# Performance work log

Hardware: AMD Instinct MI355X
Metric: run time of the kernel (lower is better)

Reference implementation:

```python
import jax, jax.numpy as jnp
import numpy as np

V, D, H = 32000, 512, 512
B, T, MAX_LEN = 32, 128, 48


def setup_inputs() -> dict:
    key = jax.random.key(0)
    ks = jax.random.split(key, 12)
    s = 0.02  # xavier-ish scale
    return {
        "inputs": jax.random.randint(ks[0], (B, 1), 0, V),
        "context": jax.random.normal(ks[1], (B, 1, H), dtype=jnp.float32),
        "max_len": MAX_LEN,
        "encoder_outputs": jax.random.normal(ks[2], (B, T, H), dtype=jnp.float32),
        "emb": jax.random.normal(ks[3], (V, D), dtype=jnp.float32) * s,
        "gru_Wih": jax.random.normal(ks[4], (3 * H, D + H), dtype=jnp.float32) * s,
        "gru_Whh": jax.random.normal(ks[5], (3 * H, H), dtype=jnp.float32) * s,
        "gru_bih": jax.random.normal(ks[6], (3 * H,), dtype=jnp.float32) * s,
        "gru_bhh": jax.random.normal(ks[7], (3 * H,), dtype=jnp.float32) * s,
        "lin_W": jax.random.normal(ks[8], (V, 2 * H), dtype=jnp.float32) * s,
        "lin_b": jax.random.normal(ks[9], (V,), dtype=jnp.float32) * s,
        "attn_W": jax.random.normal(ks[10], (H, H), dtype=jnp.float32) * s,
        "attn_b": jax.random.normal(ks[11], (H,), dtype=jnp.float32) * s,
    }


def reference(inputs, context, max_len, encoder_outputs, emb, gru_Wih, gru_Whh,
              gru_bih, gru_bhh, lin_W, lin_b, attn_W, attn_b):
    Bsz, Tlen, Hdim = encoder_outputs.shape
    ctx0 = context[:, 0, :]          # B,H  (last encoder hidden)
    e0 = emb[inputs[:, 0]]           # B,D  (start symbol embedding)
    h0 = jnp.zeros((Bsz, Hdim), dtype=context.dtype)
    # attn linear on encoder outputs is loop-invariant -> hoist
    energies = jnp.einsum('bth,gh->btg', encoder_outputs, attn_W) + attn_b  # B,T,H

    def gru_step(x, h):
        gi = x @ gru_Wih.T + gru_bih
        gh = h @ gru_Whh.T + gru_bhh
        ir, iz, inn = jnp.split(gi, 3, axis=-1)
        hr, hz, hn = jnp.split(gh, 3, axis=-1)
        r = jax.nn.sigmoid(ir + hr)
        z = jax.nn.sigmoid(iz + hz)
        n = jnp.tanh(inn + r * hn)
        return (1.0 - z) * n + z * h

    def step(carry, _):
        h, ctx, e = carry
        h = gru_step(jnp.concatenate([e, ctx], axis=-1), h)
        score = jnp.concatenate([h, ctx], axis=-1) @ lin_W.T + lin_b  # B,V
        logp = jax.nn.log_softmax(score, axis=-1)
        e_next = emb[jnp.argmax(logp, axis=-1)]                       # greedy feedback
        alpha = jax.nn.softmax(jnp.einsum('bth,bh->bt', energies, h), axis=-1)
        ctx_next = jnp.einsum('bt,bth->bh', alpha, encoder_outputs)
        return (h, ctx_next, e_next), logp

    _, logps = jax.lax.scan(step, (h0, ctx0, e0), None, length=max_len)
    # logps: (max_len, B, V) -> cat along dim1 then view => (B*max_len, V)
    return jnp.transpose(logps, (1, 0, 2)).reshape(Bsz * max_len, -1)
```

## Files before the change

### kernel.cpp

```cpp
#include <hip/hip_runtime.h>
#include <hip/hip_bf16.h>

#define V  32000
#define D  512
#define H  512
#define B  32
#define T  128
#define L  48
#define KLIN 1024
#define KGRU 1536
#define RESCUE_DELTA 0.04f
#define MAXCAND 16

typedef __attribute__((ext_vector_type(8))) short bf16x8;
typedef __attribute__((ext_vector_type(4))) float f32x4;

#define MFMA16(a, b, c) __builtin_amdgcn_mfma_f32_16x16x32_bf16(a, b, c, 0, 0, 0)

__device__ __forceinline__ void split1(float f, unsigned short* hi, unsigned short* lo) {
    unsigned u  = __float_as_uint(f);
    unsigned uh = u + (0x7FFFu + ((u >> 16) & 1u));
    unsigned short hs = (unsigned short)(uh >> 16);
    float hf = __uint_as_float(((unsigned)hs) << 16);
    float l  = f - hf;
    unsigned ul = __float_as_uint(l);
    ul += 0x7FFFu + ((ul >> 16) & 1u);
    *hi = hs;
    *lo = (unsigned short)(ul >> 16);
}

__device__ __forceinline__ void split8(const float* __restrict__ p, bf16x8& hi, bf16x8& lo) {
    float4 w0 = reinterpret_cast<const float4*>(p)[0];
    float4 w1 = reinterpret_cast<const float4*>(p)[1];
    float w[8] = {w0.x, w0.y, w0.z, w0.w, w1.x, w1.y, w1.z, w1.w};
    #pragma unroll
    for (int i = 0; i < 8; ++i) {
        unsigned u  = __float_as_uint(w[i]);
        unsigned uh = u + (0x7FFFu + ((u >> 16) & 1u));
        unsigned short hs = (unsigned short)(uh >> 16);
        float hf = __uint_as_float(((unsigned)hs) << 16);
        float l  = w[i] - hf;
        unsigned ul = __float_as_uint(l);
        ul += 0x7FFFu + ((ul >> 16) & 1u);
        hi[i] = (short)hs;
        lo[i] = (short)(ul >> 16);
    }
}

__device__ __forceinline__ void merge2(float& m1, int& i1, float& m2, int& i2,
                                       float om1, int oi1, float om2, int oi2) {
    bool ogt = (om1 > m1) || (om1 == m1 && oi1 < i1);
    float t1 = ogt ? om1 : m1; int ti1 = ogt ? oi1 : i1;
    float l1 = ogt ? m1 : om1; int li1 = ogt ? i1 : oi1;
    float w2 = ogt ? om2 : m2; int wi2 = ogt ? oi2 : i2;
    bool lgt = (l1 > w2) || (l1 == w2 && li1 < wi2);
    m1 = t1; i1 = ti1;
    m2 = lgt ? l1 : w2; i2 = lgt ? li1 : wi2;
}

__global__ void presplit_lin_hi(const float* __restrict__ src, unsigned short* __restrict__ hi)
{
    long i = (long)blockIdx.x * 256 + threadIdx.x;
    if (i >= (long)V * 128) return;
    bf16x8 h8, l8;
    split8(src + i * 8, h8, l8);
    *(bf16x8*)(hi + i * 8) = h8;
}

__global__ void presplit_gru(const float* __restrict__ Wih, const float* __restrict__ Whh,
                             unsigned short* __restrict__ hi, unsigned short* __restrict__ lo)
{
    int i = blockIdx.x * 256 + threadIdx.x;
    if (i >= 1536 * 192) return;
    int col = i / 192, k = (i % 192) * 8;
    const float* src = (k < 1024) ? (Wih + (size_t)col * 1024 + k)
                                  : (Whh + (size_t)col * 512 + (k - 1024));
    bf16x8 h8, l8;
    split8(src, h8, l8);
    *(bf16x8*)(hi + (size_t)col * KGRU + k) = h8;
    *(bf16x8*)(lo + (size_t)col * KGRU + k) = l8;
}

__global__ void init_state(const int* __restrict__ inputs, const float* __restrict__ context,
                           const float* __restrict__ emb, float* __restrict__ h_t,
                           unsigned short* __restrict__ Xghi, unsigned short* __restrict__ Xglo,
                           unsigned short* __restrict__ Xlhi, unsigned short* __restrict__ Xllo,
                           float* __restrict__ Xf)
{
    int idx = blockIdx.x * 256 + threadIdx.x;
    int b = idx >> 9, j = idx & 511;
    int tok = inputs[b];
    float e = emb[(size_t)tok * D + j];
    split1(e, &Xghi[b * KGRU + j], &Xglo[b * KGRU + j]);
    float c = context[b * H + j];
    split1(c, &Xghi[b * KGRU + 512 + j], &Xglo[b * KGRU + 512 + j]);
    split1(c, &Xlhi[b * KLIN + 512 + j], &Xllo[b * KLIN + 512 + j]);
    Xf[b * KLIN + 512 + j] = c;
    Xghi[b * KGRU + 1024 + j] = 0;
    Xglo[b * KGRU + 1024 + j] = 0;
    h_t[j * 32 + b] = 0.f;
}

__global__ void __launch_bounds__(256) energies_gemm(
    const float* __restrict__ enc, const float* __restrict__ attnW,
    const float* __restrict__ attnb, float* __restrict__ energies)
{
    int wave = threadIdx.x >> 6, lane = threadIdx.x & 63;
    int col = blockIdx.y * 64 + wave * 16 + (lane & 15);
    int kg  = (lane >> 4) * 8;
    int arow0 = blockIdx.x * 32 + (lane & 15);
    f32x4 acc0 = {0.f,0.f,0.f,0.f}, acc1 = {0.f,0.f,0.f,0.f};
    for (int k0 = 0; k0 < 512; k0 += 32) {
        bf16x8 bh, bl;   split8(attnW + (size_t)col * 512 + k0 + kg, bh, bl);
        bf16x8 a0h, a0l; split8(enc + (size_t)arow0 * 512 + k0 + kg, a0h, a0l);
        bf16x8 a1h, a1l; split8(enc + (size_t)(arow0 + 16) * 512 + k0 + kg, a1h, a1l);
        acc0 = MFMA16(a0h, bh, acc0);  acc1 = MFMA16(a1h, bh, acc1);
        acc0 = MFMA16(a0l, bh, acc0);  acc1 = MFMA16(a1l, bh, acc1);
        acc0 = MFMA16(a0h, bl, acc0);  acc1 = MFMA16(a1h, bl, acc1);
    }
    float bias = attnb[col];
    int r0 = (lane >> 4) * 4;
    #pragma unroll
    for (int i = 0; i < 4; ++i) {
        int row = blockIdx.x * 32 + r0 + i;
        energies[(size_t)row * 512 + col]        = acc0[i] + bias;
        energies[(size_t)(row + 16) * 512 + col] = acc1[i] + bias;
    }
}

__global__ void __launch_bounds__(384) gru_fused(
    const unsigned short* __restrict__ Ghi, const unsigned short* __restrict__ Glo,
    const unsigned short* __restrict__ Xghi_r, const unsigned short* __restrict__ Xglo_r,
    unsigned short* __restrict__ Xghi_w, unsigned short* __restrict__ Xglo_w,
    unsigned short* __restrict__ Xlhi_w, unsigned short* __restrict__ Xllo_w,
    float* __restrict__ Xf_w,
    const float* __restrict__ bih, const float* __restrict__ bhh,
    float* __restrict__ h_t)
{
    __shared__ float AI[3][32][16], AH[3][32][16];
    __shared__ float R[32][16], Z[32][16];
    int w = threadIdx.x >> 6, lane = threadIdx.x & 63;
    int g = (w < 3) ? w : w - 3;
    int half = (w >= 3) ? 1 : 0;
    int c = lane & 15, grp = lane >> 4, kg = grp * 8;
    int j = blockIdx.x * 16 + c;
    int gcol = g * 512 + j;
    const unsigned short* wh = Ghi + (size_t)gcol * KGRU;
    const unsigned short* wl = Glo + (size_t)gcol * KGRU;
    const unsigned short* xh = Xghi_r + (size_t)c * KGRU;
    const unsigned short* xl = Xglo_r + (size_t)c * KGRU;
    f32x4 aI0 = {0.f,0.f,0.f,0.f}, aI1 = {0.f,0.f,0.f,0.f};
    f32x4 aH0 = {0.f,0.f,0.f,0.f}, aH1 = {0.f,0.f,0.f,0.f};
    for (int k0 = half * 512; k0 < half * 512 + 512; k0 += 32) {
        bf16x8 bh = *(const bf16x8*)(wh + k0 + kg);
        bf16x8 bl = *(const bf16x8*)(wl + k0 + kg);
        bf16x8 a0h = *(const bf16x8*)(xh + k0 + kg);
        bf16x8 a0l = *(const bf16x8*)(xl + k0 + kg);
        bf16x8 a1h = *(const bf16x8*)(xh + 16 * KGRU + k0 + kg);
        bf16x8 a1l = *(const bf16x8*)(xl + 16 * KGRU + k0 + kg);
        aI0 = MFMA16(a0h, bh, aI0);  aI1 = MFMA16(a1h, bh, aI1);
        aI0 = MFMA16(a0l, bh, aI0);  aI1 = MFMA16(a1l, bh, aI1);
        aI0 = MFMA16(a0h, bl, aI0);  aI1 = MFMA16(a1h, bl, aI1);
    }
    for (int k0 = 1024 + half * 256; k0 < 1024 + half * 256 + 256; k0 += 32) {
        bf16x8 bh = *(const bf16x8*)(wh + k0 + kg);
        bf16x8 bl = *(const bf16x8*)(wl + k0 + kg);
        bf16x8 a0h = *(const bf16x8*)(xh + k0 + kg);
        bf16x8 a0l = *(const bf16x8*)(xl + k0 + kg);
        bf16x8 a1h = *(const bf16x8*)(xh + 16 * KGRU + k0 + kg);
        bf16x8 a1l = *(const bf16x8*)(xl + 16 * KGRU + k0 + kg);
        aH0 = MFMA16(a0h, bh, aH0);  aH1 = MFMA16(a1h, bh, aH1);
        aH0 = MFMA16(a0l, bh, aH0);  aH1 = MFMA16(a1l, bh, aH1);
        aH0 = MFMA16(a0h, bl, aH0);  aH1 = MFMA16(a1h, bl, aH1);
    }
    if (w >= 3) {
        #pragma unroll
        for (int i = 0; i < 4; ++i) {
            AI[g][grp * 4 + i][c] = aI0[i];  AI[g][grp * 4 + i + 16][c] = aI1[i];
            AH[g][grp * 4 + i][c] = aH0[i];  AH[g][grp * 4 + i + 16][c] = aH1[i];
        }
    }
    __syncthreads();
    float gi[8], gh[8];
    if (w < 3) {
        float bi = bih[gcol], bhv = bhh[gcol];
        #pragma unroll
        for (int i = 0; i < 4; ++i) {
            gi[i]     = aI0[i] + AI[g][grp * 4 + i][c]      + bi;
            gi[i + 4] = aI1[i] + AI[g][grp * 4 + i + 16][c] + bi;
            gh[i]     = aH0[i] + AH[g][grp * 4 + i][c]      + bhv;
            gh[i + 4] = aH1[i] + AH[g][grp * 4 + i + 16][c] + bhv;
        }
        if (w == 0) {
            #pragma unroll
            for (int i = 0; i < 8; ++i) {
                int b = (i < 4) ? grp * 4 + i : grp * 4 + (i - 4) + 16;
                R[b][c] = 1.f / (1.f + expf(-(gi[i] + gh[i])));
            }
        } else if (w == 1) {
            #pragma unroll
            for (int i = 0; i < 8; ++i) {
                int b = (i < 4) ? grp * 4 + i : grp * 4 + (i - 4) + 16;
                Z[b][c] = 1.f / (1.f + expf(-(gi[i] + gh[i])));
            }
        }
    }
    __syncthreads();
    if (w == 2) {
        float4 h0 = *(const float4*)(h_t + (size_t)j * 32 + grp * 4);
        float4 h1 = *(const float4*)(h_t + (size_t)j * 32 + grp * 4 + 16);
        float hold[8] = {h0.x, h0.y, h0.z, h0.w, h1.x, h1.y, h1.z, h1.w};
        float hn[8];
        #pragma unroll
        for (int i = 0; i < 8; ++i) {
            int b = (i < 4) ? grp * 4 + i : grp * 4 + (i - 4) + 16;
            float n = tanhf(gi[i] + R[b][c] * gh[i]);
            float z = Z[b][c];
            hn[i] = (1.f - z) * n + z * hold[i];
        }
        *(float4*)(h_t + (size_t)j * 32 + grp * 4)      = make_float4(hn[0], hn[1], hn[2], hn[3]);
        *(float4*)(h_t + (size_t)j * 32 + grp * 4 + 16) = make_float4(hn[4], hn[5], hn[6], hn[7]);
        #pragma unroll
        for (int i = 0; i < 8; ++i) {
            int b = (i < 4) ? grp * 4 + i : grp * 4 + (i - 4) + 16;
            split1(hn[i], &Xlhi_w[(size_t)b * KLIN + j], &Xllo_w[(size_t)b * KLIN + j]);
            Xf_w[(size_t)b * KLIN + j] = hn[i];
            split1(hn[i], &Xghi_w[(size_t)b * KGRU + 1024 + j], &Xglo_w[(size_t)b * KGRU + 1024 + j]);
        }
    }
}

__global__ void __launch_bounds__(256) score_attn(
    const unsigned short* __restrict__ Whi, const float* __restrict__ linb,
    const unsigned short* __restrict__ Xlhi_r, const unsigned short* __restrict__ Xllo_r,
    unsigned short* __restrict__ Xlhi_n, unsigned short* __restrict__ Xllo_n,
    float* __restrict__ Xf_n,
    unsigned short* __restrict__ Xghi_n, unsigned short* __restrict__ Xglo_n,
    const float* __restrict__ h_t, const float* __restrict__ energies,
    const float* __restrict__ enc,
    float* __restrict__ out,
    float* __restrict__ Pm, int* __restrict__ Pa,
    float* __restrict__ Pm2, int* __restrict__ Pa2,
    float* __restrict__ Ps, int t)
{
    __shared__ float Lm1[4][32], Lm2[4][32], Ls[4][32];
    __shared__ int   Li1[4][32], Li2[4][32];
    __shared__ float hrow[512], aw[128], red[256];
    int tid = threadIdx.x;
    if (blockIdx.x < 500) {
        int wave = tid >> 6, lane = tid & 63;
        int c = lane & 15, grp = lane >> 4, kg = grp * 8;
        int col = blockIdx.x * 64 + wave * 16 + c;
        const unsigned short* x0h = Xlhi_r + (size_t)c * KLIN + kg;
        const unsigned short* x0l = Xllo_r + (size_t)c * KLIN + kg;
        const unsigned short* whp = Whi + (size_t)col * KLIN + kg;
        f32x4 acc0 = {0.f,0.f,0.f,0.f}, acc1 = {0.f,0.f,0.f,0.f};
        #pragma unroll 4
        for (int k0 = 0; k0 < 1024; k0 += 32) {
            bf16x8 bh  = *(const bf16x8*)(whp + k0);
            bf16x8 a0h = *(const bf16x8*)(x0h + k0);
            bf16x8 a0l = *(const bf16x8*)(x0l + k0);
            bf16x8 a1h = *(const bf16x8*)(x0h + 16 * KLIN + k0);
            bf16x8 a1l = *(const bf16x8*)(x0l + 16 * KLIN + k0);
            acc0 = MFMA16(a0h, bh, acc0);  acc1 = MFMA16(a1h, bh, acc1);
            acc0 = MFMA16(a0l, bh, acc0);  acc1 = MFMA16(a1l, bh, acc1);
        }
        float bias = linb[col];
        float v[8];
        int r0 = grp * 4;
        #pragma unroll
        for (int i = 0; i < 4; ++i) {
            v[i]     = acc0[i] + bias;
            v[i + 4] = acc1[i] + bias;
            out[(size_t)((r0 + i) * L + t) * V + col]      = v[i];
            out[(size_t)((r0 + i + 16) * L + t) * V + col] = v[i + 4];
        }
        #pragma unroll
        for (int i = 0; i < 8; ++i) {
            float m1 = v[i]; int i1 = col; float m2 = -INFINITY; int i2 = 0x7fffffff;
            #pragma unroll
            for (int d = 1; d < 16; d <<= 1) {
                float om1 = __shfl_xor(m1, d); int oi1 = __shfl_xor(i1, d);
                float om2 = __shfl_xor(m2, d); int oi2 = __shfl_xor(i2, d);
                merge2(m1, i1, m2, i2, om1, oi1, om2, oi2);
            }
            float s = expf(v[i] - m1);
            #pragma unroll
            for (int d = 1; d < 16; d <<= 1) s += __shfl_xor(s, d);
            if (c == 0) {
                int row = (i < 4) ? r0 + i : r0 + (i - 4) + 16;
                Lm1[wave][row] = m1; Li1[wave][row] = i1;
                Lm2[wave][row] = m2; Li2[wave][row] = i2;
                Ls[wave][row] = s;
            }
        }
        __syncthreads();
        if (tid < 32) {
            float m1 = Lm1[0][tid]; int i1 = Li1[0][tid];
            float m2 = Lm2[0][tid]; int i2 = Li2[0][tid];
            #pragma unroll
            for (int q = 1; q < 4; ++q)
                merge2(m1, i1, m2, i2, Lm1[q][tid], Li1[q][tid], Lm2[q][tid], Li2[q][tid]);
            float S = 0.f;
            #pragma unroll
            for (int q = 0; q < 4; ++q) S += Ls[q][tid] * expf(Lm1[q][tid] - m1);
            Pm [tid * 500 + blockIdx.x] = m1;
            Pa [tid * 500 + blockIdx.x] = i1;
            Pm2[tid * 500 + blockIdx.x] = m2;
            Pa2[tid * 500 + blockIdx.x] = i2;
            Ps [tid * 500 + blockIdx.x] = S;
        }
    } else {
        int b = blockIdx.x - 500;
        for (int j = tid; j < 512; j += 256) hrow[j] = h_t[(size_t)j * 32 + b];
        __syncthreads();
        {
            int tt = tid >> 1, half = tid & 1;
            const float4* e4 = (const float4*)(energies + ((size_t)(b * T + tt)) * 512 + half * 256);
            const float4* h4 = (const float4*)(hrow + half * 256);
            float p = 0.f;
            #pragma unroll 4
            for (int k = 0; k < 64; ++k) {
                float4 a = e4[k], cc = h4[k];
                p += a.x * cc.x + a.y * cc.y + a.z * cc.z + a.w * cc.w;
            }
            p += __shfl_xor(p, 1);
            if (half == 0) aw[tt] = p;
        }
        __syncthreads();
        red[tid] = (tid < 128) ? aw[tid] : -INFINITY; __syncthreads();
        for (int s = 128; s > 0; s >>= 1) { if (tid < s) red[tid] = fmaxf(red[tid], red[tid + s]); __syncthreads(); }
        float am = red[0];
        __syncthreads();
        if (tid < 128) { float e = expf(aw[tid] - am); aw[tid] = e; red[tid] = e; } else red[tid] = 0.f;
        __syncthreads();
        for (int s = 128; s > 0; s >>= 1) { if (tid < s) red[tid] += red[tid + s]; __syncthreads(); }
        float asum = red[0];
        __syncthreads();
        float c0 = 0.f, c1 = 0.f;
        for (int tt2 = 0; tt2 < T; ++tt2) {
            float a = aw[tt2];
            const float* er = enc + ((size_t)(b * T + tt2)) * 512;
            c0 += a * er[tid];
            c1 += a * er[tid + 256];
        }
        c0 /= asum; c1 /= asum;
        Xf_n[(size_t)b * KLIN + 512 + tid]       = c0;
        Xf_n[(size_t)b * KLIN + 512 + tid + 256] = c1;
        split1(c0, &Xlhi_n[(size_t)b * KLIN + 512 + tid],       &Xllo_n[(size_t)b * KLIN + 512 + tid]);
        split1(c1, &Xlhi_n[(size_t)b * KLIN + 512 + tid + 256], &Xllo_n[(size_t)b * KLIN + 512 + tid + 256]);
        split1(c0, &Xghi_n[(size_t)b * KGRU + 512 + tid],       &Xglo_n[(size_t)b * KGRU + 512 + tid]);
        split1(c1, &Xghi_n[(size_t)b * KGRU + 512 + tid + 256], &Xglo_n[(size_t)b * KGRU + 512 + tid + 256]);
    }
}

__global__ void __launch_bounds__(256) finalize(
    const float* __restrict__ Pm, const int* __restrict__ Pa,
    const float* __restrict__ Pm2, const int* __restrict__ Pa2,
    const float* __restrict__ Ps,
    const float* __restrict__ linW, const float* __restrict__ linb,
    const float* __restrict__ Xf_r, const float* __restrict__ emb,
    unsigned short* __restrict__ Xghi_n, unsigned short* __restrict__ Xglo_n,
    float* __restrict__ lse_buf, int t)
{
    __shared__ float xb[1024];
    __shared__ float sred[256];
    __shared__ int   list[MAXCAND];
    __shared__ float cscore[MAXCAND];
    __shared__ int   ncand_sh, amax_sh;
    int b = blockIdx.x, tid = threadIdx.x;
    for (int j = tid; j < 1024; j += 256) xb[j] = Xf_r[(size_t)b * KLIN + j];
    if (tid == 0) ncand_sh = 0;
    __syncthreads();
    float m = -INFINITY;
    for (int i = tid; i < 500; i += 256) m = fmaxf(m, Pm[b * 500 + i]);
    sred[tid] = m; __syncthreads();
    for (int s = 128; s > 0; s >>= 1) { if (tid < s) sred[tid] = fmaxf(sred[tid], sred[tid + s]); __syncthreads(); }
    float M = sred[0];
    float thresh = M - RESCUE_DELTA;
    __syncthreads();
    float S = 0.f;
    for (int i = tid; i < 500; i += 256) {
        float pm = Pm[b * 500 + i];
        S += Ps[b * 500 + i] * expf(pm - M);
        if (pm >= thresh) { int p = atomicAdd(&ncand_sh, 1); if (p < MAXCAND) list[p] = Pa[b * 500 + i]; }
        if (Pm2[b * 500 + i] >= thresh) { int p = atomicAdd(&ncand_sh, 1); if (p < MAXCAND) list[p] = Pa2[b * 500 + i]; }
    }
    sred[tid] = S; __syncthreads();
    for (int s = 128; s > 0; s >>= 1) { if (tid < s) sred[tid] += sred[tid + s]; __syncthreads(); }
    if (tid == 0) lse_buf[b * L + t] = M + logf(sred[0]);
    __syncthreads();
    int nc = ncand_sh < MAXCAND ? ncand_sh : MAXCAND;
    int wv = tid >> 6, lane = tid & 63;
    for (int ci = wv; ci < nc; ci += 4) {
        int col = list[ci];
        const float* wr = linW + (size_t)col * 1024 + lane * 16;
        const float* xr = xb + lane * 16;
        float s = 0.f;
        #pragma unroll
        for (int jj = 0; jj < 16; jj += 4) {
            float4 a = *(const float4*)(wr + jj);
            s += a.x * xr[jj] + a.y * xr[jj + 1] + a.z * xr[jj + 2] + a.w * xr[jj + 3];
        }
        #pragma unroll
        for (int d = 1; d < 64; d <<= 1) s += __shfl_xor(s, d);
        if (lane == 0) cscore[ci] = s + linb[col];
    }
    __syncthreads();
    if (tid == 0) {
        float bm = -INFINITY; int bi = 0x7fffffff;
        for (int ci = 0; ci < nc; ++ci) {
            float vv = cscore[ci]; int cc = list[ci];
            if (vv > bm || (vv == bm && cc < bi)) { bm = vv; bi = cc; }
        }
        amax_sh = bi;
    }
    __syncthreads();
    int amax = amax_sh;
    for (int j = tid; j < 512; j += 256)
        split1(emb[(size_t)amax * D + j], &Xghi_n[(size_t)b * KGRU + j], &Xglo_n[(size_t)b * KGRU + j]);
}

__global__ void __launch_bounds__(256) subtract_lse(float* __restrict__ out,
                                                    const float* __restrict__ lse_buf)
{
    long i4 = (long)blockIdx.x * 256 + threadIdx.x;
    int row = (int)(i4 / 8000);
    float l = lse_buf[row];
    float4* p = (float4*)out + i4;
    float4 v = *p;
    v.x -= l; v.y -= l; v.z -= l; v.w -= l;
    *p = v;
}

extern "C" void kernel_launch(void* const* d_in, const int* in_sizes, int n_in,
                              void* d_out, int out_size, void* d_ws, size_t ws_size,
                              hipStream_t stream) {
    const int*   inputs  = (const int*)d_in[0];
    const float* context = (const float*)d_in[1];
    const float* enc     = (const float*)d_in[3];
    const float* emb     = (const float*)d_in[4];
    const float* Wih     = (const float*)d_in[5];
    const float* Whh     = (const float*)d_in[6];
    const float* bih     = (const float*)d_in[7];
    const float* bhh     = (const float*)d_in[8];
    const float* linW    = (const float*)d_in[9];
    const float* linb    = (const float*)d_in[10];
    const float* attnW   = (const float*)d_in[11];
    const float* attnb   = (const float*)d_in[12];
    float* out = (float*)d_out;

    char* w = (char*)d_ws;
    auto alloc = [&](size_t sz) { char* p = w; w += (sz + 255) & ~(size_t)255; return p; };
    unsigned short* Whi = (unsigned short*)alloc((size_t)V * KLIN * 2);
    unsigned short* Ghi = (unsigned short*)alloc((size_t)1536 * KGRU * 2);
    unsigned short* Glo = (unsigned short*)alloc((size_t)1536 * KGRU * 2);
    float* energies = (float*)alloc((size_t)B * T * 512 * 4);
    float* h_t      = (float*)alloc((size_t)H * B * 4);
    unsigned short* Xghi[2]; unsigned short* Xglo[2];
    unsigned short* Xlhi[2]; unsigned short* Xllo[2];
    float* Xf[2];
    for (int q = 0; q < 2; ++q) {
        Xghi[q] = (unsigned short*)alloc((size_t)B * KGRU * 2);
        Xglo[q] = (unsigned short*)alloc((size_t)B * KGRU * 2);
        Xlhi[q] = (unsigned short*)alloc((size_t)B * KLIN * 2);
        Xllo[q] = (unsigned short*)alloc((size_t)B * KLIN * 2);
        Xf[q]   = (float*)alloc((size_t)B * KLIN * 4);
    }
    float* Pm  = (float*)alloc((size_t)B * 500 * 4);
    int*   Pa  = (int*)alloc((size_t)B * 500 * 4);
    float* Pm2 = (float*)alloc((size_t)B * 500 * 4);
    int*   Pa2 = (int*)alloc((size_t)B * 500 * 4);
    float* Ps  = (float*)alloc((size_t)B * 500 * 4);
    float* lse_buf = (float*)alloc((size_t)B * L * 4);

    presplit_lin_hi<<<16000, 256, 0, stream>>>(linW, Whi);
    presplit_gru<<<1152, 256, 0, stream>>>(Wih, Whh, Ghi, Glo);
    init_state<<<64, 256, 0, stream>>>(inputs, context, emb, h_t,
                                       Xghi[0], Xglo[0], Xlhi[0], Xllo[0], Xf[0]);
    energies_gemm<<<dim3(128, 8), 256, 0, stream>>>(enc, attnW, attnb, energies);

    for (int t = 0; t < L; ++t) {
        int r = t & 1, n = (t + 1) & 1;
        gru_fused<<<32, 384, 0, stream>>>(Ghi, Glo, Xghi[r], Xglo[r],
                                          Xghi[n], Xglo[n], Xlhi[r], Xllo[r], Xf[r],
                                          bih, bhh, h_t);
        score_attn<<<532, 256, 0, stream>>>(Whi, linb, Xlhi[r], Xllo[r],
                                            Xlhi[n], Xllo[n], Xf[n],
                                            Xghi[n], Xglo[n],
                                            h_t, energies, enc, out,
                                            Pm, Pa, Pm2, Pa2, Ps, t);
        finalize<<<32, 256, 0, stream>>>(Pm, Pa, Pm2, Pa2, Ps, linW, linb,
                                         Xf[r], emb, Xghi[n], Xglo[n], lse_buf, t);
    }
    subtract_lse<<<48000, 256, 0, stream>>>(out, lse_buf);
}
```

Baseline: 4.726 ms.

## Fuse greedy argmax finalize into next step's GRU kernel

Removes the per-step finalize kernel. Each GRU block now redundantly reduces the previous step's partial max/sum buffers, rescues the argmax candidates and computes the log-sum-exp, then gathers and splits the chosen embedding rows directly inside the GRU matmul. This cuts one launch and one dependency hop per decode step. In exchange, every one of the 32 GRU blocks repeats the argmax work for all 32 batch rows, and a separate small kernel handles the final step's LSE.

```diff
diff --git a/kernel.cpp b/kernel.cpp
--- a/kernel.cpp
+++ b/kernel.cpp
@@ -81,17 +81,13 @@
     *(bf16x8*)(lo + (size_t)col * KGRU + k) = l8;
 }
 
-__global__ void init_state(const int* __restrict__ inputs, const float* __restrict__ context,
-                           const float* __restrict__ emb, float* __restrict__ h_t,
+__global__ void init_state(const float* __restrict__ context, float* __restrict__ h_t,
                            unsigned short* __restrict__ Xghi, unsigned short* __restrict__ Xglo,
                            unsigned short* __restrict__ Xlhi, unsigned short* __restrict__ Xllo,
                            float* __restrict__ Xf)
 {
     int idx = blockIdx.x * 256 + threadIdx.x;
     int b = idx >> 9, j = idx & 511;
-    int tok = inputs[b];
-    float e = emb[(size_t)tok * D + j];
-    split1(e, &Xghi[b * KGRU + j], &Xglo[b * KGRU + j]);
     float c = context[b * H + j];
     split1(c, &Xghi[b * KGRU + 512 + j], &Xglo[b * KGRU + 512 + j]);
     split1(c, &Xlhi[b * KLIN + 512 + j], &Xllo[b * KLIN + 512 + j]);
@@ -128,104 +124,192 @@
     }
 }
 
-__global__ void __launch_bounds__(384) gru_fused(
+__global__ void __launch_bounds__(384) gru_fin(
+    const int* __restrict__ inputs, const float* __restrict__ emb,
     const unsigned short* __restrict__ Ghi, const unsigned short* __restrict__ Glo,
+    const float* __restrict__ bih, const float* __restrict__ bhh,
+    const float* __restrict__ linW, const float* __restrict__ linb,
     const unsigned short* __restrict__ Xghi_r, const unsigned short* __restrict__ Xglo_r,
-    unsigned short* __restrict__ Xghi_w, unsigned short* __restrict__ Xglo_w,
+    unsigned short* __restrict__ Xghi_n, unsigned short* __restrict__ Xglo_n,
     unsigned short* __restrict__ Xlhi_w, unsigned short* __restrict__ Xllo_w,
-    float* __restrict__ Xf_w,
-    const float* __restrict__ bih, const float* __restrict__ bhh,
-    float* __restrict__ h_t)
+    float* __restrict__ Xf_w, const float* __restrict__ Xf_prev,
+    float* __restrict__ h_t,
+    const float* __restrict__ Pm, const int* __restrict__ Pa,
+    const float* __restrict__ Pm2, const int* __restrict__ Pa2,
+    const float* __restrict__ Ps,
+    float* __restrict__ lse_buf, int t)
 {
     __shared__ float AI[3][32][16], AH[3][32][16];
     __shared__ float R[32][16], Z[32][16];
-    int w = threadIdx.x >> 6, lane = threadIdx.x & 63;
-    int g = (w < 3) ? w : w - 3;
-    int half = (w >= 3) ? 1 : 0;
-    int c = lane & 15, grp = lane >> 4, kg = grp * 8;
-    int j = blockIdx.x * 16 + c;
-    int gcol = g * 512 + j;
-    const unsigned short* wh = Ghi + (size_t)gcol * KGRU;
-    const unsigned short* wl = Glo + (size_t)gcol * KGRU;
-    const unsigned short* xh = Xghi_r + (size_t)c * KGRU;
-    const unsigned short* xl = Xglo_r + (size_t)c * KGRU;
-    f32x4 aI0 = {0.f,0.f,0.f,0.f}, aI1 = {0.f,0.f,0.f,0.f};
-    f32x4 aH0 = {0.f,0.f,0.f,0.f}, aH1 = {0.f,0.f,0.f,0.f};
-    for (int k0 = half * 512; k0 < half * 512 + 512; k0 += 32) {
-        bf16x8 bh = *(const bf16x8*)(wh + k0 + kg);
-        bf16x8 bl = *(const bf16x8*)(wl + k0 + kg);
-        bf16x8 a0h = *(const bf16x8*)(xh + k0 + kg);
-        bf16x8 a0l = *(const bf16x8*)(xl + k0 + kg);
-        bf16x8 a1h = *(const bf16x8*)(xh + 16 * KGRU + k0 + kg);
-        bf16x8 a1l = *(const bf16x8*)(xl + 16 * KGRU + k0 + kg);
-        aI0 = MFMA16(a0h, bh, aI0);  aI1 = MFMA16(a1h, bh, aI1);
-        aI0 = MFMA16(a0l, bh, aI0);  aI1 = MFMA16(a1l, bh, aI1);
-        aI0 = MFMA16(a0h, bl, aI0);  aI1 = MFMA16(a1h, bl, aI1);
-    }
-    for (int k0 = 1024 + half * 256; k0 < 1024 + half * 256 + 256; k0 += 32) {
-        bf16x8 bh = *(const bf16x8*)(wh + k0 + kg);
-        bf16x8 bl = *(const bf16x8*)(wl + k0 + kg);
-        bf16x8 a0h = *(const bf16x8*)(xh + k0 + kg);
-        bf16x8 a0l = *(const bf16x8*)(xl + k0 + kg);
-        bf16x8 a1h = *(const bf16x8*)(xh + 16 * KGRU + k0 + kg);
-        bf16x8 a1l = *(const bf16x8*)(xl + 16 * KGRU + k0 + kg);
-        aH0 = MFMA16(a0h, bh, aH0);  aH1 = MFMA16(a1h, bh, aH1);
-        aH0 = MFMA16(a0l, bh, aH0);  aH1 = MFMA16(a1l, bh, aH1);
-        aH0 = MFMA16(a0h, bl, aH0);  aH1 = MFMA16(a1h, bl, aH1);
-    }
-    if (w >= 3) {
-        #pragma unroll
-        for (int i = 0; i < 4; ++i) {
-            AI[g][grp * 4 + i][c] = aI0[i];  AI[g][grp * 4 + i + 16][c] = aI1[i];
-            AH[g][grp * 4 + i][c] = aH0[i];  AH[g][grp * 4 + i + 16][c] = aH1[i];
+    __shared__ int   sAl[32];
+    __shared__ int   clist[6][MAXCAND];
+    __shared__ int   ncand[6];
+    const int tid = threadIdx.x;
+    const int w = tid >> 6, lane = tid & 63;
+
+    if (t == 0) {
+        if (tid < 32) sAl[tid] = inputs[tid];
+    } else {
+        for (int b = w; b < 32; b += 6) {
+            float m = -INFINITY; int a = 0x7fffffff;
+            for (int i = lane; i < 500; i += 64) {
+                float om = Pm[b * 500 + i]; int oa = Pa[b * 500 + i];
+                if (om > m || (om == m && oa < a)) { m = om; a = oa; }
+            }
+            #pragma unroll
+            for (int d = 1; d < 64; d <<= 1) {
+                float om = __shfl_xor(m, d); int oa = __shfl_xor(a, d);
+                if (om > m || (om == m && oa < a)) { m = om; a = oa; }
+            }
+            float M = m, thresh = M - RESCUE_DELTA;
+            if (lane == 0) ncand[w] = 0;
+            float S = 0.f;
+            for (int i = lane; i < 500; i += 64) {
+                float pm = Pm[b * 500 + i];
+                S += Ps[b * 500 + i] * expf(pm - M);
+                if (pm >= thresh) { int p = atomicAdd(&ncand[w], 1); if (p < MAXCAND) clist[w][p] = Pa[b * 500 + i]; }
+                if (Pm2[b * 500 + i] >= thresh) { int p = atomicAdd(&ncand[w], 1); if (p < MAXCAND) clist[w][p] = Pa2[b * 500 + i]; }
+            }
+            #pragma unroll
+            for (int d = 1; d < 64; d <<= 1) S += __shfl_xor(S, d);
+            if (blockIdx.x == 0 && lane == 0) lse_buf[b * L + (t - 1)] = M + logf(S);
+            int nc = ncand[w]; nc = nc < MAXCAND ? nc : MAXCAND;
+            float best = -INFINITY; int bi = 0x7fffffff;
+            for (int ci = 0; ci < nc; ++ci) {
+                int col = clist[w][ci];
+                const float* wr = linW + (size_t)col * 1024 + lane * 16;
+                const float* xr = Xf_prev + (size_t)b * KLIN + lane * 16;
+                float s = 0.f;
+                #pragma unroll
+                for (int jj = 0; jj < 16; jj += 4) {
+                    float4 av = *(const float4*)(wr + jj);
+                    float4 xv = *(const float4*)(xr + jj);
+                    s += av.x * xv.x + av.y * xv.y + av.z * xv.z + av.w * xv.w;
+                }
+                #pragma unroll
+                for (int d = 1; d < 64; d <<= 1) s += __shfl_xor(s, d);
+                s += linb[col];
+                if (s > best || (s == best && col < bi)) { best = s; bi = col; }
+            }
+            if (lane == 0) sAl[b] = bi;
         }
     }
     __syncthreads();
-    float gi[8], gh[8];
-    if (w < 3) {
-        float bi = bih[gcol], bhv = bhh[gcol];
-        #pragma unroll
-        for (int i = 0; i < 4; ++i) {
-            gi[i]     = aI0[i] + AI[g][grp * 4 + i][c]      + bi;
-            gi[i + 4] = aI1[i] + AI[g][grp * 4 + i + 16][c] + bi;
-            gh[i]     = aH0[i] + AH[g][grp * 4 + i][c]      + bhv;
-            gh[i + 4] = aH1[i] + AH[g][grp * 4 + i + 16][c] + bhv;
-        }
-        if (w == 0) {
+
+    {
+        int g = (w < 3) ? w : w - 3;
+        int c = lane & 15, grp = lane >> 4, kg = grp * 8;
+        int j = blockIdx.x * 16 + c;
+        int gcol = g * 512 + j;
+        const unsigned short* wh = Ghi + (size_t)gcol * KGRU;
+        const unsigned short* wl = Glo + (size_t)gcol * KGRU;
+        const unsigned short* xh = Xghi_r + (size_t)c * KGRU;
+        const unsigned short* xl = Xglo_r + (size_t)c * KGRU;
+        f32x4 aI0 = {0.f,0.f,0.f,0.f}, aI1 = {0.f,0.f,0.f,0.f};
+        f32x4 aH0 = {0.f,0.f,0.f,0.f}, aH1 = {0.f,0.f,0.f,0.f};
+        if (w < 3) {
+            const float* e0p = emb + (size_t)sAl[c] * 512;
+            const float* e1p = emb + (size_t)sAl[c + 16] * 512;
+            for (int k0 = 0; k0 < 512; k0 += 32) {
+                bf16x8 bh = *(const bf16x8*)(wh + k0 + kg);
+                bf16x8 bl = *(const bf16x8*)(wl + k0 + kg);
+                bf16x8 a0h, a0l, a1h, a1l;
+                split8(e0p + k0 + kg, a0h, a0l);
+                split8(e1p + k0 + kg, a1h, a1l);
+                aI0 = MFMA16(a0h, bh, aI0);  aI1 = MFMA16(a1h, bh, aI1);
+                aI0 = MFMA16(a0l, bh, aI0);  aI1 = MFMA16(a1l, bh, aI1);
+                aI0 = MFMA16(a0h, bl, aI0);  aI1 = MFMA16(a1h, bl, aI1);
+            }
+            for (int k0 = 1024; k0 < 1280; k0 += 32) {
+                bf16x8 bh = *(const bf16x8*)(wh + k0 + kg);
+                bf16x8 bl = *(const bf16x8*)(wl + k0 + kg);
+                bf16x8 a0h = *(const bf16x8*)(xh + k0 + kg);
+                bf16x8 a0l = *(const bf16x8*)(xl + k0 + kg);
+                bf16x8 a1h = *(const bf16x8*)(xh + 16 * KGRU + k0 + kg);
+                bf16x8 a1l = *(const bf16x8*)(xl + 16 * KGRU + k0 + kg);
+                aH0 = MFMA16(a0h, bh, aH0);  aH1 = MFMA16(a1h, bh, aH1);
+                aH0 = MFMA16(a0l, bh, aH0);  aH1 = MFMA16(a1l, bh, aH1);
+                aH0 = MFMA16(a0h, bl, aH0);  aH1 = MFMA16(a1h, bl, aH1);
+            }
+        } else {
+            for (int k0 = 512; k0 < 1024; k0 += 32) {
+                bf16x8 bh = *(const bf16x8*)(wh + k0 + kg);
+                bf16x8 bl = *(const bf16x8*)(wl + k0 + kg);
+                bf16x8 a0h = *(const bf16x8*)(xh + k0 + kg);
+                bf16x8 a0l = *(const bf16x8*)(xl + k0 + kg);
+                bf16x8 a1h = *(const bf16x8*)(xh + 16 * KGRU + k0 + kg);
+                bf16x8 a1l = *(const bf16x8*)(xl + 16 * KGRU + k0 + kg);
+                aI0 = MFMA16(a0h, bh, aI0);  aI1 = MFMA16(a1h, bh, aI1);
+                aI0 = MFMA16(a0l, bh, aI0);  aI1 = MFMA16(a1l, bh, aI1);
+                aI0 = MFMA16(a0h, bl, aI0);  aI1 = MFMA16(a1h, bl, aI1);
+            }
+            for (int k0 = 1280; k0 < 1536; k0 += 32) {
+                bf16x8 bh = *(const bf16x8*)(wh + k0 + kg);
+                bf16x8 bl = *(const bf16x8*)(wl + k0 + kg);
+                bf16x8 a0h = *(const bf16x8*)(xh + k0 + kg);
+                bf16x8 a0l = *(const bf16x8*)(xl + k0 + kg);
+                bf16x8 a1h = *(const bf16x8*)(xh + 16 * KGRU + k0 + kg);
+                bf16x8 a1l = *(const bf16x8*)(xl + 16 * KGRU + k0 + kg);
+                aH0 = MFMA16(a0h, bh, aH0);  aH1 = MFMA16(a1h, bh, aH1);
+                aH0 = MFMA16(a0l, bh, aH0);  aH1 = MFMA16(a1l, bh, aH1);
+                aH0 = MFMA16(a0h, bl, aH0);  aH1 = MFMA16(a1h, bl, aH1);
+            }
+        }
+        if (w >= 3) {
+            #pragma unroll
+            for (int i = 0; i < 4; ++i) {
+                AI[g][grp * 4 + i][c] = aI0[i];  AI[g][grp * 4 + i + 16][c] = aI1[i];
+                AH[g][grp * 4 + i][c] = aH0[i];  AH[g][grp * 4 + i + 16][c] = aH1[i];
+            }
+        }
+        __syncthreads();
+        float gi[8], gh[8];
+        if (w < 3) {
+            float bi = bih[gcol], bhv = bhh[gcol];
+            #pragma unroll
+            for (int i = 0; i < 4; ++i) {
+                gi[i]     = aI0[i] + AI[g][grp * 4 + i][c]      + bi;
+                gi[i + 4] = aI1[i] + AI[g][grp * 4 + i + 16][c] + bi;
+                gh[i]     = aH0[i] + AH[g][grp * 4 + i][c]      + bhv;
+                gh[i + 4] = aH1[i] + AH[g][grp * 4 + i + 16][c] + bhv;
+            }
+            if (w == 0) {
+                #pragma unroll
+                for (int i = 0; i < 8; ++i) {
+                    int b = (i < 4) ? grp * 4 + i : grp * 4 + (i - 4) + 16;
+                    R[b][c] = 1.f / (1.f + expf(-(gi[i] + gh[i])));
+                }
+            } else if (w == 1) {
+                #pragma unroll
+                for (int i = 0; i < 8; ++i) {
+                    int b = (i < 4) ? grp * 4 + i : grp * 4 + (i - 4) + 16;
+                    Z[b][c] = 1.f / (1.f + expf(-(gi[i] + gh[i])));
+                }
+            }
+        }
+        __syncthreads();
+        if (w == 2) {
+            int j2 = j;
+            float4 h0 = *(const float4*)(h_t + (size_t)j2 * 32 + grp * 4);
+            float4 h1 = *(const float4*)(h_t + (size_t)j2 * 32 + grp * 4 + 16);
+            float hold[8] = {h0.x, h0.y, h0.z, h0.w, h1.x, h1.y, h1.z, h1.w};
+            float hn[8];
             #pragma unroll
             for (int i = 0; i < 8; ++i) {
                 int b = (i < 4) ? grp * 4 + i : grp * 4 + (i - 4) + 16;
-                R[b][c] = 1.f / (1.f + expf(-(gi[i] + gh[i])));
-            }
-        } else if (w == 1) {
+                float n = tanhf(gi[i] + R[b][c] * gh[i]);
+                float z = Z[b][c];
+                hn[i] = (1.f - z) * n + z * hold[i];
+            }
+            *(float4*)(h_t + (size_t)j2 * 32 + grp * 4)      = make_float4(hn[0], hn[1], hn[2], hn[3]);
+            *(float4*)(h_t + (size_t)j2 * 32 + grp * 4 + 16) = make_float4(hn[4], hn[5], hn[6], hn[7]);
             #pragma unroll
             for (int i = 0; i < 8; ++i) {
                 int b = (i < 4) ? grp * 4 + i : grp * 4 + (i - 4) + 16;
-                Z[b][c] = 1.f / (1.f + expf(-(gi[i] + gh[i])));
-            }
-        }
-    }
-    __syncthreads();
-    if (w == 2) {
-        float4 h0 = *(const float4*)(h_t + (size_t)j * 32 + grp * 4);
-        float4 h1 = *(const float4*)(h_t + (size_t)j * 32 + grp * 4 + 16);
-        float hold[8] = {h0.x, h0.y, h0.z, h0.w, h1.x, h1.y, h1.z, h1.w};
-        float hn[8];
-        #pragma unroll
-        for (int i = 0; i < 8; ++i) {
-            int b = (i < 4) ? grp * 4 + i : grp * 4 + (i - 4) + 16;
-            float n = tanhf(gi[i] + R[b][c] * gh[i]);
-            float z = Z[b][c];
-            hn[i] = (1.f - z) * n + z * hold[i];
-        }
-        *(float4*)(h_t + (size_t)j * 32 + grp * 4)      = make_float4(hn[0], hn[1], hn[2], hn[3]);
-        *(float4*)(h_t + (size_t)j * 32 + grp * 4 + 16) = make_float4(hn[4], hn[5], hn[6], hn[7]);
-        #pragma unroll
-        for (int i = 0; i < 8; ++i) {
-            int b = (i < 4) ? grp * 4 + i : grp * 4 + (i - 4) + 16;
-            split1(hn[i], &Xlhi_w[(size_t)b * KLIN + j], &Xllo_w[(size_t)b * KLIN + j]);
-            Xf_w[(size_t)b * KLIN + j] = hn[i];
-            split1(hn[i], &Xghi_w[(size_t)b * KGRU + 1024 + j], &Xglo_w[(size_t)b * KGRU + 1024 + j]);
+                split1(hn[i], &Xlhi_w[(size_t)b * KLIN + j2], &Xllo_w[(size_t)b * KLIN + j2]);
+                Xf_w[(size_t)b * KLIN + j2] = hn[i];
+                split1(hn[i], &Xghi_n[(size_t)b * KGRU + 1024 + j2], &Xglo_n[(size_t)b * KGRU + 1024 + j2]);
+            }
         }
     }
 }
@@ -354,71 +438,22 @@
     }
 }
 
-__global__ void __launch_bounds__(256) finalize(
-    const float* __restrict__ Pm, const int* __restrict__ Pa,
-    const float* __restrict__ Pm2, const int* __restrict__ Pa2,
-    const float* __restrict__ Ps,
-    const float* __restrict__ linW, const float* __restrict__ linb,
-    const float* __restrict__ Xf_r, const float* __restrict__ emb,
-    unsigned short* __restrict__ Xghi_n, unsigned short* __restrict__ Xglo_n,
-    float* __restrict__ lse_buf, int t)
-{
-    __shared__ float xb[1024];
+__global__ void __launch_bounds__(256) lse47(
+    const float* __restrict__ Pm, const float* __restrict__ Ps, float* __restrict__ lse_buf)
+{
     __shared__ float sred[256];
-    __shared__ int   list[MAXCAND];
-    __shared__ float cscore[MAXCAND];
-    __shared__ int   ncand_sh, amax_sh;
     int b = blockIdx.x, tid = threadIdx.x;
-    for (int j = tid; j < 1024; j += 256) xb[j] = Xf_r[(size_t)b * KLIN + j];
-    if (tid == 0) ncand_sh = 0;
-    __syncthreads();
     float m = -INFINITY;
     for (int i = tid; i < 500; i += 256) m = fmaxf(m, Pm[b * 500 + i]);
     sred[tid] = m; __syncthreads();
     for (int s = 128; s > 0; s >>= 1) { if (tid < s) sred[tid] = fmaxf(sred[tid], sred[tid + s]); __syncthreads(); }
     float M = sred[0];
-    float thresh = M - RESCUE_DELTA;
     __syncthreads();
     float S = 0.f;
-    for (int i = tid; i < 500; i += 256) {
-        float pm = Pm[b * 500 + i];
-        S += Ps[b * 500 + i] * expf(pm - M);
-        if (pm >= thresh) { int p = atomicAdd(&ncand_sh, 1); if (p < MAXCAND) list[p] = Pa[b * 500 + i]; }
-        if (Pm2[b * 500 + i] >= thresh) { int p = atomicAdd(&ncand_sh, 1); if (p < MAXCAND) list[p] = Pa2[b * 500 + i]; }
-    }
+    for (int i = tid; i < 500; i += 256) S += Ps[b * 500 + i] * expf(Pm[b * 500 + i] - M);
     sred[tid] = S; __syncthreads();
     for (int s = 128; s > 0; s >>= 1) { if (tid < s) sred[tid] += sred[tid + s]; __syncthreads(); }
-    if (tid == 0) lse_buf[b * L + t] = M + logf(sred[0]);
-    __syncthreads();
-    int nc = ncand_sh < MAXCAND ? ncand_sh : MAXCAND;
-    int wv = tid >> 6, lane = tid & 63;
-    for (int ci = wv; ci < nc; ci += 4) {
-        int col = list[ci];
-        const float* wr = linW + (size_t)col * 1024 + lane * 16;
-        const float* xr = xb + lane * 16;
-        float s = 0.f;
-        #pragma unroll
-        for (int jj = 0; jj < 16; jj += 4) {
-            float4 a = *(const float4*)(wr + jj);
-            s += a.x * xr[jj] + a.y * xr[jj + 1] + a.z * xr[jj + 2] + a.w * xr[jj + 3];
-        }
-        #pragma unroll
-        for (int d = 1; d < 64; d <<= 1) s += __shfl_xor(s, d);
-        if (lane == 0) cscore[ci] = s + linb[col];
-    }
-    __syncthreads();
-    if (tid == 0) {
-        float bm = -INFINITY; int bi = 0x7fffffff;
-        for (int ci = 0; ci < nc; ++ci) {
-            float vv = cscore[ci]; int cc = list[ci];
-            if (vv > bm || (vv == bm && cc < bi)) { bm = vv; bi = cc; }
-        }
-        amax_sh = bi;
-    }
-    __syncthreads();
-    int amax = amax_sh;
-    for (int j = tid; j < 512; j += 256)
-        split1(emb[(size_t)amax * D + j], &Xghi_n[(size_t)b * KGRU + j], &Xglo_n[(size_t)b * KGRU + j]);
+    if (tid == 0) lse_buf[b * L + 47] = M + logf(sred[0]);
 }
 
 __global__ void __launch_bounds__(256) subtract_lse(float* __restrict__ out,
@@ -476,22 +511,24 @@
 
     presplit_lin_hi<<<16000, 256, 0, stream>>>(linW, Whi);
     presplit_gru<<<1152, 256, 0, stream>>>(Wih, Whh, Ghi, Glo);
-    init_state<<<64, 256, 0, stream>>>(inputs, context, emb, h_t,
+    init_state<<<64, 256, 0, stream>>>(context, h_t,
                                        Xghi[0], Xglo[0], Xlhi[0], Xllo[0], Xf[0]);
     energies_gemm<<<dim3(128, 8), 256, 0, stream>>>(enc, attnW, attnb, energies);
 
     for (int t = 0; t < L; ++t) {
-        int r = t & 1, n = (t + 1) & 1;
-        gru_fused<<<32, 384, 0, stream>>>(Ghi, Glo, Xghi[r], Xglo[r],
-                                          Xghi[n], Xglo[n], Xlhi[r], Xllo[r], Xf[r],
-                                          bih, bhh, h_t);
-        score_attn<<<532, 256, 0, stream>>>(Whi, linb, Xlhi[r], Xllo[r],
-                                            Xlhi[n], Xllo[n], Xf[n],
-                                            Xghi[n], Xglo[n],
-                                            h_t, energies, enc, out,
-                                            Pm, Pa, Pm2, Pa2, Ps, t);
-        finalize<<<32, 256, 0, stream>>>(Pm, Pa, Pm2, Pa2, Ps, linW, linb,
-                                         Xf[r], emb, Xghi[n], Xglo[n], lse_buf, t);
-    }
+        int r = t & 1, n = 1 - r;
+        gru_fin<<<32, 384, 0, stream>>>(
+            inputs, emb, Ghi, Glo, bih, bhh, linW, linb,
+            Xghi[r], Xglo[r], Xghi[n], Xglo[n],
+            Xlhi[r], Xllo[r], Xf[r], Xf[n],
+            h_t, Pm, Pa, Pm2, Pa2, Ps, lse_buf, t);
+        score_attn<<<532, 256, 0, stream>>>(
+            Whi, linb, Xlhi[r], Xllo[r],
+            Xlhi[n], Xllo[n], Xf[n],
+            Xghi[n], Xglo[n],
+            h_t, energies, enc, out,
+            Pm, Pa, Pm2, Pa2, Ps, t);
+    }
+    lse47<<<32, 256, 0, stream>>>(Pm, Ps, lse_buf);
     subtract_lse<<<48000, 256, 0, stream>>>(out, lse_buf);
 }
```

After: 8.466 ms. +79.1%, slower.
